# Performance work log

Measured on AMD Instinct MI355X. Metric: run time of the kernel, lower is better.

The kernel has to match this reference:

```python
import jax, jax.numpy as jnp
import numpy as np

QKV = 1024   # qkv_size (input feature dim)
E = 64       # embed_size (per-head dim)
H = 16       # num_heads
OUT = 1024   # output_size
B, S = 8, 1024


def setup_inputs() -> dict:
    key = jax.random.key(0)
    ks = jax.random.split(key, 8)
    inv = 1.0 / np.sqrt(QKV)
    return {
        "query": jax.random.normal(ks[0], (B, S, QKV), jnp.float32),
        "key": jax.random.normal(ks[1], (B, S, QKV), jnp.float32),
        "value": jax.random.normal(ks[2], (B, S, QKV), jnp.float32),
        # stacked per-head projection weights, torch Linear convention y = x @ W.T -> store as [H, QKV, E]
        "Wq": jax.random.normal(ks[3], (H, QKV, E), jnp.float32) * inv,
        "Wk": jax.random.normal(ks[4], (H, QKV, E), jnp.float32) * inv,
        "Wv": jax.random.normal(ks[5], (H, QKV, E), jnp.float32) * inv,
        "Wo": jax.random.normal(ks[6], (OUT, H * E), jnp.float32) / np.sqrt(H * E),
        "bo": jax.random.normal(ks[7], (OUT,), jnp.float32) * 0.01,
    }


def reference(query, key, value, Wq, Wk, Wv, Wo, bo):
    # batched over heads: [B,S,QKV] x [H,QKV,E] -> [B,H,S,E]
    Q = jnp.einsum("bsd,hde->bhse", query, Wq)
    K = jnp.einsum("bsd,hde->bhse", key, Wk)
    V = jnp.einsum("bsd,hde->bhse", value, Wv)
    # NOTE: original scales by sqrt(qkv_dim) (input dim), not per-head dim
    scale = 1.0 / jnp.sqrt(jnp.float32(QKV))
    scores = jnp.einsum("bhse,bhte->bhst", Q, K) * scale  # [B,H,S,S]
    attn = jax.nn.softmax(scores, axis=-1)
    attended = jnp.einsum("bhst,bhte->bhse", attn, V)     # [B,H,S,E]
    # concat heads along last dim (head-major order matches torch.cat of head outputs)
    concat = attended.transpose(0, 2, 1, 3).reshape(query.shape[0], query.shape[1], H * E)
    return concat @ Wo.T + bo
```

## Files before the change

### kernel.cpp

```cpp
#include <hip/hip_runtime.h>
#include <stdint.h>


typedef __bf16 bf16x8 __attribute__((ext_vector_type(8)));
typedef float f32x4 __attribute__((ext_vector_type(4)));

typedef __attribute__((address_space(3))) uint32_t lds_u32;
typedef const __attribute__((address_space(1))) uint32_t glb_u32;

__device__ __forceinline__ ushort f2bf(float f) {
  uint32_t x = __float_as_uint(f);
  x += 0x7fff + ((x >> 16) & 1);
  return (ushort)(x >> 16);
}
__device__ __forceinline__ bf16x8 ld8(const ushort* p) {
  union { uint4 u; bf16x8 b; } c;
  c.u = *reinterpret_cast<const uint4*>(p);
  return c.b;
}
__device__ __forceinline__ void cvt16(const float* __restrict__ src,
                                      ushort* __restrict__ dst) {
  union { uint4 u[2]; ushort s[16]; } o;
#pragma unroll
  for (int i = 0; i < 4; ++i) {
    const float4 f = reinterpret_cast<const float4*>(src)[i];
    o.s[4 * i + 0] = f2bf(f.x);
    o.s[4 * i + 1] = f2bf(f.y);
    o.s[4 * i + 2] = f2bf(f.z);
    o.s[4 * i + 3] = f2bf(f.w);
  }
  reinterpret_cast<uint4*>(dst)[0] = o.u[0];
  reinterpret_cast<uint4*>(dst)[1] = o.u[1];
}

__device__ __forceinline__ void gld16(const ushort* g, ushort* l) {
  __builtin_amdgcn_global_load_lds((glb_u32*)g, (lds_u32*)l, 16, 0, 0);
}

__global__ __launch_bounds__(256) void prep_wt3(
    const float* __restrict__ W0, const float* __restrict__ W1,
    const float* __restrict__ W2, ushort* __restrict__ T0,
    ushort* __restrict__ T1, ushort* __restrict__ T2) {
  __shared__ __align__(16) ushort tile[64 * 72];
  const int sel = blockIdx.x >> 8;
  const float* W = sel == 0 ? W0 : sel == 1 ? W1 : W2;
  ushort* WT = sel == 0 ? T0 : sel == 1 ? T1 : T2;
  const int bid = blockIdx.x & 255;
  const int h = bid >> 4;
  const int kt = bid & 15;
  const int t = threadIdx.x;
  const int row = t >> 2;
  const int ch = (t & 3) * 16;
  cvt16(W + ((size_t)h * 1024 + kt * 64 + row) * 64 + ch, &tile[row * 72 + ch]);
  __syncthreads();
  const int e = t >> 2;
  const int kc = (t & 3) * 16;
  ushort vals[16];
#pragma unroll
  for (int j = 0; j < 16; ++j) vals[j] = tile[(kc + j) * 72 + e];
  ushort* dst = WT + (size_t)(h * 64 + e) * 1024 + kt * 64 + kc;
  reinterpret_cast<uint4*>(dst)[0] = *reinterpret_cast<uint4*>(&vals[0]);
  reinterpret_cast<uint4*>(dst)[1] = *reinterpret_cast<uint4*>(&vals[8]);
}

__global__ __launch_bounds__(256) void cvt3(const float* __restrict__ s0,
                                            ushort* __restrict__ d0,
                                            const float* __restrict__ s1,
                                            ushort* __restrict__ d1,
                                            const float* __restrict__ s2,
                                            ushort* __restrict__ d2) {
  int b = blockIdx.x;
  const float* s;
  ushort* d;
  if (b < 2048) { s = s0; d = d0; }
  else if (b < 4096) { s = s1; d = d1; b -= 2048; }
  else { s = s2; d = d2; b -= 4096; }
  const int i = (b * 256 + threadIdx.x) * 16;
  cvt16(s + i, d + i);
}

template <bool F32OUT>
__device__ __forceinline__ void core_bb(ushort* __restrict__ As,
                                        ushort* __restrict__ Bs,
                                        const ushort* __restrict__ A,
                                        const ushort* __restrict__ Bt,
                                        const float* __restrict__ bias,
                                        void* __restrict__ Cv, float oscale,
                                        int bx, int by) {
  const int n0 = bx * 128;
  const int m0 = by * 128;
  const int t = threadIdx.x;
  const int lane = t & 63;
  const int w = t >> 6;
  const int wm = w >> 1, wn = w & 1;
  const int col = lane & 15;
  const int quad = lane >> 4;
  const int gr = lane >> 3;
  const int gc = (lane & 7) * 8;

  f32x4 acc[4][4];
#pragma unroll
  for (int i = 0; i < 4; ++i)
#pragma unroll
    for (int j = 0; j < 4; ++j) acc[i][j] = (f32x4){0.f, 0.f, 0.f, 0.f};

  const ushort* a_src = A + (size_t)(m0 + w * 8 + gr) * 1024 + gc;
  const ushort* b_src = Bt + (size_t)(n0 + w * 8 + gr) * 1024 + gc;
  ushort* as_base = &As[(w * 8) * 64];
  ushort* bs_base = &Bs[(w * 8) * 64];

  for (int k0 = 0; k0 < 1024; k0 += 64) {
#pragma unroll
    for (int c = 0; c < 4; ++c) {
      gld16(a_src + (size_t)c * 32 * 1024 + k0, as_base + c * 32 * 64);
      gld16(b_src + (size_t)c * 32 * 1024 + k0, bs_base + c * 32 * 64);
    }
    __syncthreads();

#pragma unroll
    for (int half = 0; half < 2; ++half) {
      bf16x8 af[4], bfr[4];
#pragma unroll
      for (int i = 0; i < 4; ++i)
        af[i] = ld8(&As[(wm * 64 + i * 16 + col) * 64 + half * 32 + quad * 8]);
#pragma unroll
      for (int j = 0; j < 4; ++j)
        bfr[j] = ld8(&Bs[(wn * 64 + j * 16 + col) * 64 + half * 32 + quad * 8]);
#pragma unroll
      for (int i = 0; i < 4; ++i)
#pragma unroll
        for (int j = 0; j < 4; ++j)
          acc[i][j] = __builtin_amdgcn_mfma_f32_16x16x32_bf16(af[i], bfr[j],
                                                              acc[i][j], 0, 0, 0);
    }
    __syncthreads();
  }

#pragma unroll
  for (int i = 0; i < 4; ++i)
#pragma unroll
    for (int j = 0; j < 4; ++j) {
      const int n = n0 + wn * 64 + j * 16 + col;
      float bv = 0.f;
      if (F32OUT) bv = bias[n];
#pragma unroll
      for (int r = 0; r < 4; ++r) {
        const int m = m0 + wm * 64 + i * 16 + quad * 4 + r;
        if (F32OUT)
          reinterpret_cast<float*>(Cv)[(size_t)m * 1024 + n] = acc[i][j][r] + bv;
        else
          reinterpret_cast<ushort*>(Cv)[(size_t)m * 1024 + n] =
              f2bf(acc[i][j][r] * oscale);
      }
    }
}

__device__ __forceinline__ void core_f32a(ushort* __restrict__ As72,
                                          ushort* __restrict__ Bs,
                                          const float* __restrict__ A,
                                          const ushort* __restrict__ Bt,
                                          ushort* __restrict__ C, int bx,
                                          int by) {
  const int n0 = bx * 128;
  const int m0 = by * 128;
  const int t = threadIdx.x;
  const int lane = t & 63;
  const int w = t >> 6;
  const int wm = w >> 1, wn = w & 1;
  const int col = lane & 15;
  const int quad = lane >> 4;
  const int gr = lane >> 3;
  const int gc = (lane & 7) * 8;
  const int srow = t >> 1;
  const int sc0 = (t & 1) * 32;

  f32x4 acc[4][4];
#pragma unroll
  for (int i = 0; i < 4; ++i)
#pragma unroll
    for (int j = 0; j < 4; ++j) acc[i][j] = (f32x4){0.f, 0.f, 0.f, 0.f};

  const float* a_src = A + (size_t)(m0 + srow) * 1024 + sc0;
  const ushort* b_src = Bt + (size_t)(n0 + w * 8 + gr) * 1024 + gc;
  ushort* bs_base = &Bs[(w * 8) * 64];

  for (int k0 = 0; k0 < 1024; k0 += 64) {
#pragma unroll
    for (int c = 0; c < 4; ++c)
      gld16(b_src + (size_t)c * 32 * 1024 + k0, bs_base + c * 32 * 64);
    cvt16(a_src + k0, &As72[srow * 72 + sc0]);
    cvt16(a_src + k0 + 16, &As72[srow * 72 + sc0 + 16]);
    __syncthreads();

#pragma unroll
    for (int half = 0; half < 2; ++half) {
      bf16x8 af[4], bfr[4];
#pragma unroll
      for (int i = 0; i < 4; ++i)
        af[i] = ld8(&As72[(wm * 64 + i * 16 + col) * 72 + half * 32 + quad * 8]);
#pragma unroll
      for (int j = 0; j < 4; ++j)
        bfr[j] = ld8(&Bs[(wn * 64 + j * 16 + col) * 64 + half * 32 + quad * 8]);
#pragma unroll
      for (int i = 0; i < 4; ++i)
#pragma unroll
        for (int j = 0; j < 4; ++j)
          acc[i][j] = __builtin_amdgcn_mfma_f32_16x16x32_bf16(af[i], bfr[j],
                                                              acc[i][j], 0, 0, 0);
    }
    __syncthreads();
  }

#pragma unroll
  for (int i = 0; i < 4; ++i)
#pragma unroll
    for (int j = 0; j < 4; ++j) {
      const int n = n0 + wn * 64 + j * 16 + col;
#pragma unroll
      for (int r = 0; r < 4; ++r) {
        const int m = m0 + wm * 64 + i * 16 + quad * 4 + r;
        C[(size_t)m * 1024 + n] = f2bf(acc[i][j][r]);
      }
    }
}

__global__ __launch_bounds__(256) void gemm_out(const ushort* __restrict__ A,
                                                const ushort* __restrict__ Bt,
                                                const float* __restrict__ bias,
                                                float* __restrict__ C) {
  __shared__ __align__(16) ushort As[128 * 64];
  __shared__ __align__(16) ushort Bs[128 * 64];
  const int id = blockIdx.x;
  const int bx = (id >> 3) & 7;
  const int by = ((id >> 6) << 3) | (id & 7);
  core_bb<true>(As, Bs, A, Bt, bias, C, 1.0f, bx, by);
}

__global__ __launch_bounds__(256) void gemm_proj3(
    const ushort* __restrict__ Aq, const ushort* __restrict__ Bq,
    ushort* __restrict__ Cq, const ushort* __restrict__ Ak,
    const ushort* __restrict__ Bk, ushort* __restrict__ Ck,
    const float* __restrict__ Av, const ushort* __restrict__ Bv,
    ushort* __restrict__ Cvp) {
  __shared__ __align__(16) ushort As[128 * 72];
  __shared__ __align__(16) ushort Bs[128 * 64];
  const int id = blockIdx.x;
  const int bx = (id >> 3) & 7;
  const int by = ((id >> 6) << 3) | (id & 7);
  if (by < 64)
    core_bb<false>(As, Bs, Aq, Bq, nullptr, Cq, 0.03125f, bx, by);
  else if (by < 128)
    core_bb<false>(As, Bs, Ak, Bk, nullptr, Ck, 1.0f, bx, by - 64);
  else
    core_f32a(As, Bs, Av, Bv, Cvp, bx, by - 128);
}

__global__ __launch_bounds__(256) void flash_attn(const ushort* __restrict__ Q,
                                                  const ushort* __restrict__ K,
                                                  const ushort* __restrict__ V,
                                                  ushort* __restrict__ O) {
  __shared__ __align__(16) ushort QP[128 * 72];
  __shared__ __align__(16) ushort Ks[64 * 64];
  __shared__ __align__(16) ushort Vt[64 * 72];
  const int pair = blockIdx.x & 127;
  const int b = pair >> 4;
  const int h = pair & 15;
  const int qt = blockIdx.x >> 7;
  const int t = threadIdx.x;
  const int lane = t & 63;
  const int w = t >> 6;
  const int col = lane & 15;
  const int quad = lane >> 4;

  const size_t base = (size_t)b * 1024 * 1024 + h * 64;
  const int qrow0 = qt * 128;

  {
    const int row = t >> 1;
    const int c0 = (t & 1) * 32;
    const ushort* src = Q + base + (size_t)(qrow0 + row) * 1024 + c0;
    uint4 v0 = reinterpret_cast<const uint4*>(src)[0];
    uint4 v1 = reinterpret_cast<const uint4*>(src)[1];
    uint4 v2 = reinterpret_cast<const uint4*>(src)[2];
    uint4 v3 = reinterpret_cast<const uint4*>(src)[3];
    reinterpret_cast<uint4*>(&QP[row * 72 + c0])[0] = v0;
    reinterpret_cast<uint4*>(&QP[row * 72 + c0])[1] = v1;
    reinterpret_cast<uint4*>(&QP[row * 72 + c0])[2] = v2;
    reinterpret_cast<uint4*>(&QP[row * 72 + c0])[3] = v3;
  }
  __syncthreads();
  bf16x8 qa[2][2];
#pragma unroll
  for (int g = 0; g < 2; ++g)
#pragma unroll
    for (int half = 0; half < 2; ++half)
      qa[g][half] =
          ld8(&QP[(w * 32 + g * 16 + col) * 72 + half * 32 + quad * 8]);

  f32x4 o_[2][4];
#pragma unroll
  for (int g = 0; g < 2; ++g)
#pragma unroll
    for (int c = 0; c < 4; ++c) o_[g][c] = (f32x4){0.f, 0.f, 0.f, 0.f};
  float m_s[2] = {-1e30f, -1e30f};
  float l_s[2] = {0.f, 0.f};

  const int krow = w * 16 + (lane >> 3);
  const int kcs = (((lane & 7) ^ (lane >> 3)) << 3);
  const int s7 = col & 7;

  for (int kt = 0; kt < 16; ++kt) {
    {
      const ushort* k0 = K + base + (size_t)(kt * 64 + krow) * 1024 + kcs;
      gld16(k0, &Ks[(w * 16) * 64]);
      gld16(k0 + 8 * 1024, &Ks[(w * 16 + 8) * 64]);
      const int vs = t & 63;
      const int ve = (t >> 6) * 16;
      const ushort* vsrc = V + base + (size_t)(kt * 64 + vs) * 1024 + ve;
      union { uint4 u[2]; ushort s[16]; } vv;
      vv.u[0] = reinterpret_cast<const uint4*>(vsrc)[0];
      vv.u[1] = reinterpret_cast<const uint4*>(vsrc)[1];
#pragma unroll
      for (int j = 0; j < 16; ++j) Vt[(ve + j) * 72 + vs] = vv.s[j];
    }
    __syncthreads();

    f32x4 sc[2][4];
#pragma unroll
    for (int c = 0; c < 4; ++c) {
      const int R = (c * 16 + col) * 64;
      bf16x8 kb0 = ld8(&Ks[R + ((quad ^ s7) << 3)]);
      bf16x8 kb1 = ld8(&Ks[R + (((quad + 4) ^ s7) << 3)]);
#pragma unroll
      for (int g = 0; g < 2; ++g) {
        f32x4 z = {0.f, 0.f, 0.f, 0.f};
        z = __builtin_amdgcn_mfma_f32_16x16x32_bf16(kb0, qa[g][0], z, 0, 0, 0);
        z = __builtin_amdgcn_mfma_f32_16x16x32_bf16(kb1, qa[g][1], z, 0, 0, 0);
        sc[g][c] = z;
      }
    }

    float al[2];
    bool df[2];
#pragma unroll
    for (int g = 0; g < 2; ++g) {
      float mx = sc[g][0][0];
#pragma unroll
      for (int c = 0; c < 4; ++c)
#pragma unroll
        for (int r = 0; r < 4; ++r) mx = fmaxf(mx, sc[g][c][r]);
      mx = fmaxf(mx, __shfl_xor(mx, 16));
      mx = fmaxf(mx, __shfl_xor(mx, 32));
      df[g] = __all(mx - m_s[g] <= 8.0f) != 0;
      if (df[g]) {
        al[g] = 1.0f;
      } else {
        const float m_new = fmaxf(m_s[g], mx);
        al[g] = __expf(m_s[g] - m_new);
        m_s[g] = m_new;
      }
      float rs = 0.f;
      const int prow = (w * 32 + g * 16 + col) * 72;
#pragma unroll
      for (int c = 0; c < 4; ++c) {
        const float p0 = __expf(sc[g][c][0] - m_s[g]);
        const float p1 = __expf(sc[g][c][1] - m_s[g]);
        const float p2 = __expf(sc[g][c][2] - m_s[g]);
        const float p3 = __expf(sc[g][c][3] - m_s[g]);
        rs += (p0 + p1) + (p2 + p3);
        union { uint2 u; ushort s[4]; } pk;
        pk.s[0] = f2bf(p0);
        pk.s[1] = f2bf(p1);
        pk.s[2] = f2bf(p2);
        pk.s[3] = f2bf(p3);
        *reinterpret_cast<uint2*>(&QP[prow + c * 16 + quad * 4]) = pk.u;
      }
      rs += __shfl_xor(rs, 16);
      rs += __shfl_xor(rs, 32);
      l_s[g] = df[g] ? (l_s[g] + rs) : (l_s[g] * al[g] + rs);
    }

#pragma unroll
    for (int g = 0; g < 2; ++g)
      if (!df[g]) {
#pragma unroll
        for (int r = 0; r < 4; ++r) {
          const float a = __shfl(al[g], (lane & 48) | (quad * 4 + r));
          o_[g][0][r] *= a;
          o_[g][1][r] *= a;
          o_[g][2][r] *= a;
          o_[g][3][r] *= a;
        }
      }

    bf16x8 pa[2][2];
#pragma unroll
    for (int g = 0; g < 2; ++g)
#pragma unroll
      for (int half = 0; half < 2; ++half)
        pa[g][half] =
            ld8(&QP[(w * 32 + g * 16 + col) * 72 + half * 32 + quad * 8]);
#pragma unroll
    for (int c = 0; c < 4; ++c) {
      bf16x8 vb0 = ld8(&Vt[(c * 16 + col) * 72 + quad * 8]);
      bf16x8 vb1 = ld8(&Vt[(c * 16 + col) * 72 + 32 + quad * 8]);
#pragma unroll
      for (int g = 0; g < 2; ++g) {
        o_[g][c] = __builtin_amdgcn_mfma_f32_16x16x32_bf16(pa[g][0], vb0,
                                                           o_[g][c], 0, 0, 0);
        o_[g][c] = __builtin_amdgcn_mfma_f32_16x16x32_bf16(pa[g][1], vb1,
                                                           o_[g][c], 0, 0, 0);
      }
    }
    __syncthreads();
  }

#pragma unroll
  for (int g = 0; g < 2; ++g)
#pragma unroll
    for (int r = 0; r < 4; ++r) {
      const float lr = __shfl(l_s[g], (lane & 48) | (quad * 4 + r));
      const float inv = 1.f / lr;
      const size_t row =
          base + (size_t)(qrow0 + w * 32 + g * 16 + quad * 4 + r) * 1024;
      O[row + 0 + col] = f2bf(o_[g][0][r] * inv);
      O[row + 16 + col] = f2bf(o_[g][1][r] * inv);
      O[row + 32 + col] = f2bf(o_[g][2][r] * inv);
      O[row + 48 + col] = f2bf(o_[g][3][r] * inv);
    }
}

extern "C" void kernel_launch(void* const* d_in, const int* in_sizes, int n_in,
                              void* d_out, int out_size, void* d_ws, size_t ws_size,
                              hipStream_t stream) {
  const float* q = (const float*)d_in[0];
  const float* k = (const float*)d_in[1];
  const float* v = (const float*)d_in[2];
  const float* Wq = (const float*)d_in[3];
  const float* Wk = (const float*)d_in[4];
  const float* Wv = (const float*)d_in[5];
  const float* Wo = (const float*)d_in[6];
  const float* bo = (const float*)d_in[7];
  float* out = (float*)d_out;
  ushort* ws = (ushort*)d_ws;

  const size_t M8 = 8u << 20;
  const size_t M1 = 1u << 20;
  ushort* Qp = ws;
  ushort* Kp = ws + M8;
  ushort* Vp = ws + 2 * M8;
  ushort* WqT = ws + 3 * M8;
  ushort* WkT = WqT + M1;
  ushort* WvT = WkT + M1;
  ushort* WoB = WvT + M1;

  ushort* X0 = (ushort*)d_out;
  ushort* X1 = X0 + M8;

  prep_wt3<<<768, 256, 0, stream>>>(Wq, Wk, Wv, WqT, WkT, WvT);
  cvt3<<<4352, 256, 0, stream>>>(q, X0, k, X1, Wo, WoB);
  gemm_proj3<<<1536, 256, 0, stream>>>(X0, WqT, Qp, X1, WkT, Kp, v, WvT, Vp);

  flash_attn<<<1024, 256, 0, stream>>>(Qp, Kp, Vp, Qp);

  gemm_out<<<512, 256, 0, stream>>>(Qp, WoB, bo, out);
}
```

Before: 352.4 us.

## Double-buffer LDS tiles in bf16 GEMM cores to overlap loads with MFMA

Replaces the single-buffered bf16 GEMM main loop with a two-stage ping-pong pipeline. The next K tile is issued as global-to-LDS loads while MFMAs run on the current tile, using explicit vmcnt waits and s_barriers. This is meant to hide global load latency in the projection and output GEMMs. It doubles LDS use to 64KB per block, which may lower occupancy, and the hand-tuned waitcnt logic is fragile.

```diff
diff --git a/kernel.cpp b/kernel.cpp
--- a/kernel.cpp
+++ b/kernel.cpp
@@ -79,14 +79,26 @@
   cvt16(s + i, d + i);
 }
 
+__device__ __forceinline__ void stage8(const ushort* a_src, const ushort* b_src,
+                                       ushort* as, ushort* bs, int w, int k0) {
+#pragma unroll
+  for (int c = 0; c < 4; ++c) {
+    gld16(a_src + (size_t)c * 32 * 1024 + k0, as + (w * 8 + c * 32) * 64);
+    gld16(b_src + (size_t)c * 32 * 1024 + k0, bs + (w * 8 + c * 32) * 64);
+  }
+}
+
 template <bool F32OUT>
-__device__ __forceinline__ void core_bb(ushort* __restrict__ As,
-                                        ushort* __restrict__ Bs,
-                                        const ushort* __restrict__ A,
-                                        const ushort* __restrict__ Bt,
-                                        const float* __restrict__ bias,
-                                        void* __restrict__ Cv, float oscale,
-                                        int bx, int by) {
+__device__ __forceinline__ void core_bb_pipe(ushort* __restrict__ S,
+                                             const ushort* __restrict__ A,
+                                             const ushort* __restrict__ Bt,
+                                             const float* __restrict__ bias,
+                                             void* __restrict__ Cv,
+                                             float oscale, int bx, int by) {
+  ushort* A0 = S;
+  ushort* B0 = S + 128 * 64;
+  ushort* A1 = S + 2 * 128 * 64;
+  ushort* B1 = S + 3 * 128 * 64;
   const int n0 = bx * 128;
   const int m0 = by * 128;
   const int t = threadIdx.x;
@@ -106,26 +118,17 @@
 
   const ushort* a_src = A + (size_t)(m0 + w * 8 + gr) * 1024 + gc;
   const ushort* b_src = Bt + (size_t)(n0 + w * 8 + gr) * 1024 + gc;
-  ushort* as_base = &As[(w * 8) * 64];
-  ushort* bs_base = &Bs[(w * 8) * 64];
-
-  for (int k0 = 0; k0 < 1024; k0 += 64) {
-#pragma unroll
-    for (int c = 0; c < 4; ++c) {
-      gld16(a_src + (size_t)c * 32 * 1024 + k0, as_base + c * 32 * 64);
-      gld16(b_src + (size_t)c * 32 * 1024 + k0, bs_base + c * 32 * 64);
-    }
-    __syncthreads();
-
+
+  auto compute = [&](const ushort* asb, const ushort* bsb) {
 #pragma unroll
     for (int half = 0; half < 2; ++half) {
       bf16x8 af[4], bfr[4];
 #pragma unroll
       for (int i = 0; i < 4; ++i)
-        af[i] = ld8(&As[(wm * 64 + i * 16 + col) * 64 + half * 32 + quad * 8]);
+        af[i] = ld8(&asb[(wm * 64 + i * 16 + col) * 64 + half * 32 + quad * 8]);
 #pragma unroll
       for (int j = 0; j < 4; ++j)
-        bfr[j] = ld8(&Bs[(wn * 64 + j * 16 + col) * 64 + half * 32 + quad * 8]);
+        bfr[j] = ld8(&bsb[(wn * 64 + j * 16 + col) * 64 + half * 32 + quad * 8]);
 #pragma unroll
       for (int i = 0; i < 4; ++i)
 #pragma unroll
@@ -133,7 +136,34 @@
           acc[i][j] = __builtin_amdgcn_mfma_f32_16x16x32_bf16(af[i], bfr[j],
                                                               acc[i][j], 0, 0, 0);
     }
-    __syncthreads();
+  };
+
+  stage8(a_src, b_src, A0, B0, w, 0);
+
+  for (int t2 = 0; t2 < 16; t2 += 2) {
+    stage8(a_src, b_src, A1, B1, w, (t2 + 1) * 64);
+    asm volatile("s_waitcnt vmcnt(8)" ::: "memory");
+    __builtin_amdgcn_sched_barrier(0);
+    __builtin_amdgcn_s_barrier();
+    __builtin_amdgcn_sched_barrier(0);
+    compute(A0, B0);
+    asm volatile("s_waitcnt lgkmcnt(0)" ::: "memory");
+    __builtin_amdgcn_sched_barrier(0);
+    __builtin_amdgcn_s_barrier();
+
+    if (t2 < 14) {
+      stage8(a_src, b_src, A0, B0, w, (t2 + 2) * 64);
+      asm volatile("s_waitcnt vmcnt(8)" ::: "memory");
+    } else {
+      asm volatile("s_waitcnt vmcnt(0)" ::: "memory");
+    }
+    __builtin_amdgcn_sched_barrier(0);
+    __builtin_amdgcn_s_barrier();
+    __builtin_amdgcn_sched_barrier(0);
+    compute(A1, B1);
+    asm volatile("s_waitcnt lgkmcnt(0)" ::: "memory");
+    __builtin_amdgcn_sched_barrier(0);
+    __builtin_amdgcn_s_barrier();
   }
 
 #pragma unroll
@@ -155,12 +185,13 @@
     }
 }
 
-__device__ __forceinline__ void core_f32a(ushort* __restrict__ As72,
-                                          ushort* __restrict__ Bs,
+__device__ __forceinline__ void core_f32a(ushort* __restrict__ S,
                                           const float* __restrict__ A,
                                           const ushort* __restrict__ Bt,
                                           ushort* __restrict__ C, int bx,
                                           int by) {
+  ushort* As72 = S;
+  ushort* Bs = S + 128 * 72;
   const int n0 = bx * 128;
   const int m0 = by * 128;
   const int t = threadIdx.x;
@@ -228,12 +259,11 @@
                                                 const ushort* __restrict__ Bt,
                                                 const float* __restrict__ bias,
                                                 float* __restrict__ C) {
-  __shared__ __align__(16) ushort As[128 * 64];
-  __shared__ __align__(16) ushort Bs[128 * 64];
+  __shared__ __align__(16) ushort S[4 * 128 * 64];
   const int id = blockIdx.x;
   const int bx = (id >> 3) & 7;
   const int by = ((id >> 6) << 3) | (id & 7);
-  core_bb<true>(As, Bs, A, Bt, bias, C, 1.0f, bx, by);
+  core_bb_pipe<true>(S, A, Bt, bias, C, 1.0f, bx, by);
 }
 
 __global__ __launch_bounds__(256) void gemm_proj3(
@@ -242,17 +272,16 @@
     const ushort* __restrict__ Bk, ushort* __restrict__ Ck,
     const float* __restrict__ Av, const ushort* __restrict__ Bv,
     ushort* __restrict__ Cvp) {
-  __shared__ __align__(16) ushort As[128 * 72];
-  __shared__ __align__(16) ushort Bs[128 * 64];
+  __shared__ __align__(16) ushort S[4 * 128 * 64];
   const int id = blockIdx.x;
   const int bx = (id >> 3) & 7;
   const int by = ((id >> 6) << 3) | (id & 7);
   if (by < 64)
-    core_bb<false>(As, Bs, Aq, Bq, nullptr, Cq, 0.03125f, bx, by);
+    core_bb_pipe<false>(S, Aq, Bq, nullptr, Cq, 0.03125f, bx, by);
   else if (by < 128)
-    core_bb<false>(As, Bs, Ak, Bk, nullptr, Ck, 1.0f, bx, by - 64);
+    core_bb_pipe<false>(S, Ak, Bk, nullptr, Ck, 1.0f, bx, by - 64);
   else
-    core_f32a(As, Bs, Av, Bv, Cvp, bx, by - 128);
+    core_f32a(S, Av, Bv, Cvp, bx, by - 128);
 }
 
 __global__ __launch_bounds__(256) void flash_attn(const ushort* __restrict__ Q,
```

Measured after the change: 341.6 us. 3.1% less time.
